# Kernel optimization log

Measured on AMD Instinct MI355X. Metric: run time of the kernel, lower is better.

Reference implementation:

```python
import jax, jax.numpy as jnp
import numpy as np

N_NODES = 50000

def _add_self_loops(edge_index, n):
    loop = jnp.arange(n, dtype=edge_index.dtype)
    src = jnp.concatenate([edge_index[0], loop])
    dst = jnp.concatenate([edge_index[1], loop])
    return src, dst

def _gcn_conv(x, src, dst, W, b, n):
    h = x @ W
    deg = jax.ops.segment_sum(jnp.ones_like(dst, dtype=h.dtype), dst, num_segments=n)
    inv_sqrt = jnp.where(deg > 0, jax.lax.rsqrt(deg), 0.0)
    coef = inv_sqrt[src] * inv_sqrt[dst]            # [E]
    msg = h[src] * coef[:, None]                     # [E, hidden]
    return jax.ops.segment_sum(msg, dst, num_segments=n) + b

def _gat_conv(x, src, dst, W, att_src, att_dst, b, n, heads, out_dim):
    # PyG GATConv, concat=False -> mean over heads; self-loops already added
    h = (x @ W).reshape(n, heads, out_dim)           # [N, H, F]
    a_src = jnp.sum(h * att_src, axis=-1)            # [N, H]
    a_dst = jnp.sum(h * att_dst, axis=-1)            # [N, H]
    e = a_src[src] + a_dst[dst]                      # [E, H]
    e = jax.nn.leaky_relu(e, negative_slope=0.2)
    # neighborhood softmax over edges grouped by destination
    m = jax.ops.segment_max(e, dst, num_segments=n)  # [N, H]
    ex = jnp.exp(e - m[dst])
    denom = jax.ops.segment_sum(ex, dst, num_segments=n)
    alpha = ex / denom[dst]                          # [E, H]
    out = jax.ops.segment_sum(h[src] * alpha[:, :, None], dst, num_segments=n)  # [N, H, F]
    return out.mean(axis=1) + b                      # concat=False -> head mean

def setup_inputs() -> dict:
    key = jax.random.key(0)
    ks = jax.random.split(key, 12)
    n, input_dim, hidden, output_dim, heads = N_NODES, 128, 128, 64, 2
    gat_out = hidden // 2
    x = jax.random.normal(ks[0], (n, input_dim), dtype=jnp.float32)
    edge_index = jax.random.randint(ks[1], (2, 800000), 0, n, dtype=jnp.int64)
    s = lambda fi, fo: float(np.sqrt(1.0 / fi))
    W1 = jax.random.normal(ks[2], (input_dim, hidden), dtype=jnp.float32) * s(input_dim, hidden)
    b1 = jnp.zeros((hidden,), dtype=jnp.float32)
    Wg = jax.random.normal(ks[3], (hidden, heads * gat_out), dtype=jnp.float32) * s(hidden, gat_out)
    att_src = jax.random.normal(ks[4], (heads, gat_out), dtype=jnp.float32) * s(gat_out, 1)
    att_dst = jax.random.normal(ks[5], (heads, gat_out), dtype=jnp.float32) * s(gat_out, 1)
    bg = jnp.zeros((gat_out,), dtype=jnp.float32)
    W3 = jax.random.normal(ks[6], (gat_out, output_dim), dtype=jnp.float32) * s(gat_out, output_dim)
    b3 = jnp.zeros((output_dim,), dtype=jnp.float32)
    return {"x": x, "edge_index": edge_index, "W1": W1, "b1": b1, "Wg": Wg,
            "att_src": att_src, "att_dst": att_dst, "bg": bg, "W3": W3, "b3": b3}

def reference(x, edge_index, W1, b1, Wg, att_src, att_dst, bg, W3, b3):
    n = x.shape[0]
    heads, gat_out = att_src.shape
    src, dst = _add_self_loops(edge_index, n)
    # dropout is identity in eval mode
    h = _gcn_conv(x, src, dst, W1, b1, n)
    h = jax.nn.relu(h)
    h = _gat_conv(h, src, dst, Wg, att_src, att_dst, bg, n, heads, gat_out)
    h = jax.nn.elu(h)
    return _gcn_conv(h, src, dst, W3, b3, n)
```

## Files before the change

kernel.cpp:

```cpp
#include <hip/hip_runtime.h>
#include <hip/hip_bf16.h>
#include <math.h>

#define N_NODES 50000
#define E0      800000
#define E_TOT   (E0 + N_NODES)
#define SCAP    512

using bf16 = __hip_bfloat16;
typedef __attribute__((ext_vector_type(8))) short bfrag;
typedef __attribute__((ext_vector_type(4))) float ffrag;

static __device__ __forceinline__ float bfu2f_lo(unsigned u){ return __uint_as_float(u << 16); }
static __device__ __forceinline__ float bfu2f_hi(unsigned u){ return __uint_as_float(u & 0xffff0000u); }

static __device__ __forceinline__ unsigned packbf(float a, float b){
    bf16 x = __float2bfloat16(a), y = __float2bfloat16(b);
    unsigned short ux = *reinterpret_cast<unsigned short*>(&x);
    unsigned short uy = *reinterpret_cast<unsigned short*>(&y);
    return ((unsigned)uy << 16) | ux;
}

static __device__ __forceinline__ int detect_f32(const unsigned* xu){
    int lane = threadIdx.x & 63;
    unsigned ex = (xu[lane] >> 7) & 0xFF;
    return (__ballot(ex < 100 || ex > 140) != 0ULL);
}
static __device__ __forceinline__ int detect_i32(const int* ei){
    int lane = threadIdx.x & 63;
    return (__ballot(ei[2 * lane + 1] != 0) != 0ULL);
}

static __device__ __forceinline__ float ldany(const void* p, int i, int isf32){
    return isf32 ? ((const float*)p)[i] : __bfloat162float(((const bf16*)p)[i]);
}

__global__ void k_convert(const void* __restrict__ xv,
                          const void* W1, const void* Wg, const void* W3,
                          const void* b1, const void* bg, const void* b3,
                          const void* as_, const void* ad_,
                          bf16* __restrict__ W1p, bf16* __restrict__ Wgp,
                          bf16* __restrict__ W3p, float* __restrict__ vecf,
                          bf16* __restrict__ xb, int* __restrict__ deg){
    const int NXB = (N_NODES * 32 + 255) / 256;
    int b = blockIdx.x, t = threadIdx.x;
    if (b >= 148 + NXB){
        int i = (b - 148 - NXB) * 256 + t;
        if (i < N_NODES) deg[i] = 0;
        return;
    }
    int isf = detect_f32((const unsigned*)xv);
    if (b >= 148){
        int i = (b - 148) * 256 + t;
        if (i < N_NODES * 32){
            if (isf){
                float4 v = ((const float4*)xv)[i];
                ((uint2*)xb)[i] = make_uint2(packbf(v.x, v.y), packbf(v.z, v.w));
            } else {
                ((uint2*)xb)[i] = ((const uint2*)xv)[i];
            }
        }
        return;
    }
    if (b < 16){
        int dd = b * 256 + t;
        int j  = dd & 7;
        int L  = (dd >> 3) & 63;
        int kc = (dd >> 9) & 1;
        int ct = dd >> 10;
        int k = kc * 32 + ((L >> 4) << 3) + j;
        int n = ct * 16 + (L & 15);
        W3p[dd] = __float2bfloat16(ldany(W3, k * 64 + n, isf));
    }
    else if (b < 18){
        int i = (b - 16) * 256 + t;
        float v;
        if      (i < 128) v = ldany(b1,  i,       isf);
        else if (i < 192) v = ldany(bg,  i - 128, isf);
        else if (i < 256) v = ldany(b3,  i - 192, isf);
        else if (i < 384) v = ldany(as_, i - 256, isf);
        else              v = ldany(ad_, i - 384, isf);
        vecf[i] = v;
    } else {
        int d = (b - 18) * 256 + t;
        const void* Wsrc = (d < 16384) ? W1 : Wg;
        bf16* Wdst = (d < 16384) ? W1p : Wgp;
        int dd = d & 16383;
        int j  = dd & 7;
        int L  = (dd >> 3) & 63;
        int kc = (dd >> 9) & 3;
        int ct = dd >> 11;
        int k = kc * 32 + ((L >> 4) << 3) + j;
        int n = ct * 16 + (L & 15);
        Wdst[dd] = __float2bfloat16(ldany(Wsrc, k * 128 + n, isf));
    }
}


static __device__ __forceinline__ int load_dst(const int* ei, int e, int is32){
    if (e >= E0) return e - E0;
    return is32 ? ei[E0 + e] : (int)((const long long*)ei)[E0 + e];
}
static __device__ __forceinline__ int load_src(const int* ei, int e, int is32){
    if (e >= E0) return e - E0;
    return is32 ? ei[e] : (int)((const long long*)ei)[e];
}

__global__ void k_count(const int* __restrict__ ei, int* __restrict__ deg,
                        int2* __restrict__ pkrk){
    int is32 = detect_i32(ei);
    int e = blockIdx.x * blockDim.x + threadIdx.x;
    if (e >= E_TOT) return;
    int dst = load_dst(ei, e, is32);
    int src = load_src(ei, e, is32);
    if ((unsigned)dst >= N_NODES || (unsigned)src >= N_NODES){
        pkrk[e] = make_int2(-1, 0);
        return;
    }
    int r = atomicAdd(&deg[dst], 1);
    pkrk[e] = make_int2((src << 16) | dst, r);
}

__global__ void k_scanA(const int* __restrict__ deg, int* __restrict__ tmp, int* __restrict__ blk){
    __shared__ int s[256];
    int t = threadIdx.x;
    int i = blockIdx.x * 256 + t;
    int v = (i < N_NODES) ? deg[i] : 0;
    s[t] = v; __syncthreads();
    for (int off = 1; off < 256; off <<= 1){
        int x = (t >= off) ? s[t - off] : 0;
        __syncthreads();
        s[t] += x;
        __syncthreads();
    }
    if (t == 255) blk[blockIdx.x] = s[255];
    if (i < N_NODES) tmp[i] = s[t] - v;
}

__global__ void k_scanC(int* __restrict__ row_ptr, const int* __restrict__ blk,
                        const int* __restrict__ deg, float* __restrict__ inv_sqrt,
                        int nb){
    __shared__ int s[256];
    int t = threadIdx.x;
    int B = blockIdx.x;
    s[t] = (t < nb && t < B) ? blk[t] : 0;
    __syncthreads();
    for (int off = 128; off; off >>= 1){
        if (t < off) s[t] += s[t + off];
        __syncthreads();
    }
    int base = s[0];
    int i = B * 256 + t;
    if (i < N_NODES){
        row_ptr[i] += base;
        int d = deg[i];
        inv_sqrt[i] = (d > 0) ? rsqrtf((float)d) : 0.0f;
    }
    if (i == 0) row_ptr[N_NODES] = E_TOT;
}

__global__ void k_fill(const int2* __restrict__ pkrk, const int* __restrict__ row_ptr,
                       const float* __restrict__ isq, int2* __restrict__ ecr){
    int e = blockIdx.x * blockDim.x + threadIdx.x;
    if (e >= E_TOT) return;
    int2 pr = pkrk[e];
    unsigned pk = (unsigned)pr.x;
    if (pk == 0xFFFFFFFFu) return;
    int dst = pk & 0xFFFF;
    int src = pk >> 16;
    int pos = row_ptr[dst] + pr.y;
    float c = isq[dst] * isq[src];
    ecr[pos] = make_int2(src, __float_as_int(c));
}

__global__ __launch_bounds__(256) void k_gather(
        const uint4* __restrict__ xb16, const int* __restrict__ rp,
        const int2* __restrict__ ecr, uint4* __restrict__ Xa16){
    __shared__ int   scsr[SCAP];
    __shared__ float scf[SCAP];
    int n0 = blockIdx.x * 4;
    int b0 = rp[n0];
    int stot = min(rp[n0 + 4] - b0, SCAP);
    for (int i = threadIdx.x; i < stot; i += 256){
        int2 ev = ecr[b0 + i];
        scsr[i] = ev.x;
        scf[i]  = __int_as_float(ev.y);
    }
    __syncthreads();

    int w = threadIdx.x >> 6, lane = threadIdx.x & 63;
    int q4 = lane >> 4, fz = lane & 15;
    int n = n0 + w;
    float a0=0,a1=0,a2=0,a3=0,a4=0,a5=0,a6=0,a7=0;
    int b = rp[n] - b0, e = rp[n + 1] - b0;
    int elim = min(e, stot);
    #pragma unroll 2
    for (int i = b + q4; i < elim; i += 4){
        int s = scsr[i];
        float c = scf[i];
        uint4 v = xb16[(size_t)s * 16 + fz];
        a0 += c * bfu2f_lo(v.x);  a1 += c * bfu2f_hi(v.x);
        a2 += c * bfu2f_lo(v.y);  a3 += c * bfu2f_hi(v.y);
        a4 += c * bfu2f_lo(v.z);  a5 += c * bfu2f_hi(v.z);
        a6 += c * bfu2f_lo(v.w);  a7 += c * bfu2f_hi(v.w);
    }
    int start = max(b, stot);
    int i0 = start + (((b + q4) - start) & 3);
    for (int i = i0; i < e; i += 4){
        int2 ev = ecr[b0 + i];
        float c = __int_as_float(ev.y);
        uint4 v = xb16[(size_t)ev.x * 16 + fz];
        a0 += c * bfu2f_lo(v.x);  a1 += c * bfu2f_hi(v.x);
        a2 += c * bfu2f_lo(v.y);  a3 += c * bfu2f_hi(v.y);
        a4 += c * bfu2f_lo(v.z);  a5 += c * bfu2f_hi(v.z);
        a6 += c * bfu2f_lo(v.w);  a7 += c * bfu2f_hi(v.w);
    }
    a0 += __shfl_xor(a0, 32, 64);  a0 += __shfl_xor(a0, 16, 64);
    a1 += __shfl_xor(a1, 32, 64);  a1 += __shfl_xor(a1, 16, 64);
    a2 += __shfl_xor(a2, 32, 64);  a2 += __shfl_xor(a2, 16, 64);
    a3 += __shfl_xor(a3, 32, 64);  a3 += __shfl_xor(a3, 16, 64);
    a4 += __shfl_xor(a4, 32, 64);  a4 += __shfl_xor(a4, 16, 64);
    a5 += __shfl_xor(a5, 32, 64);  a5 += __shfl_xor(a5, 16, 64);
    a6 += __shfl_xor(a6, 32, 64);  a6 += __shfl_xor(a6, 16, 64);
    a7 += __shfl_xor(a7, 32, 64);  a7 += __shfl_xor(a7, 16, 64);
    if (lane < 16){
        uint4 o;
        o.x = packbf(a0, a1);  o.y = packbf(a2, a3);
        o.z = packbf(a4, a5);  o.w = packbf(a6, a7);
        Xa16[(size_t)n * 16 + fz] = o;
    }
}

template<int EPI>
__global__ __launch_bounds__(512) void k_gemm_mfma(
        const bf16* __restrict__ A, const bf16* __restrict__ Wp,
        const float* __restrict__ vecf, bf16* __restrict__ O,
        float2* __restrict__ aS, float2* __restrict__ aD){
    int wid  = threadIdx.x >> 6;
    int lane = threadIdx.x & 63;
    int r0 = blockIdx.x * 128 + wid * 16;
    int m = lane & 15, q = lane >> 4;

    const bfrag* Ap = (const bfrag*)(A + (size_t)(r0 + m) * 128);
    bfrag af[4];
    #pragma unroll
    for (int kc = 0; kc < 4; ++kc) af[kc] = Ap[kc * 4 + q];

    ffrag c[8];
    #pragma unroll
    for (int ct = 0; ct < 8; ++ct){
        const bfrag* Bp = (const bfrag*)Wp + ct * 256 + lane;
        ffrag acc = {0.f, 0.f, 0.f, 0.f};
        #pragma unroll
        for (int kc = 0; kc < 4; ++kc)
            acc = __builtin_amdgcn_mfma_f32_16x16x32_bf16(af[kc], Bp[kc * 64], acc, 0, 0, 0);
        c[ct] = acc;
    }

    if (EPI == 0){
        #pragma unroll
        for (int ct = 0; ct < 8; ++ct){
            int col = ct * 16 + m;
            float bb = vecf[col];
            #pragma unroll
            for (int r = 0; r < 4; ++r){
                int row = r0 + q * 4 + r;
                if (row < N_NODES)
                    O[(size_t)row * 128 + col] = __float2bfloat16(fmaxf(c[ct][r] + bb, 0.f));
            }
        }
    } else {
        float ps0[4] = {0,0,0,0}, ps1[4] = {0,0,0,0};
        float pd0[4] = {0,0,0,0}, pd1[4] = {0,0,0,0};
        #pragma unroll
        for (int ct = 0; ct < 8; ++ct){
            const int h = ct >> 2;
            int f = (ct & 3) * 16 + m;
            float as_v = vecf[256 + h * 64 + f];
            float ad_v = vecf[384 + h * 64 + f];
            #pragma unroll
            for (int r = 0; r < 4; ++r){
                int row = r0 + q * 4 + r;
                if (row < N_NODES)
                    O[(size_t)row * 128 + f * 2 + h] = __float2bfloat16(c[ct][r]);
                if (h == 0){ ps0[r] += c[ct][r] * as_v;  pd0[r] += c[ct][r] * ad_v; }
                else       { ps1[r] += c[ct][r] * as_v;  pd1[r] += c[ct][r] * ad_v; }
            }
        }
        #pragma unroll
        for (int off = 1; off < 16; off <<= 1){
            #pragma unroll
            for (int r = 0; r < 4; ++r){
                ps0[r] += __shfl_xor(ps0[r], off, 64);
                ps1[r] += __shfl_xor(ps1[r], off, 64);
                pd0[r] += __shfl_xor(pd0[r], off, 64);
                pd1[r] += __shfl_xor(pd1[r], off, 64);
            }
        }
        if (m == 0){
            #pragma unroll
            for (int r = 0; r < 4; ++r){
                int row = r0 + q * 4 + r;
                if (row < N_NODES){
                    aS[row] = make_float2(ps0[r], ps1[r]);
                    aD[row] = make_float2(pd0[r], pd1[r]);
                }
            }
        }
    }
}

__global__ __launch_bounds__(256) void k_gemm_z(
        const bf16* __restrict__ Y, const bf16* __restrict__ W3p,
        bf16* __restrict__ Z){
    int wid  = threadIdx.x >> 6;
    int lane = threadIdx.x & 63;
    int r0 = blockIdx.x * 64 + wid * 16;
    int m = lane & 15, q = lane >> 4;

    const bfrag* Ap = (const bfrag*)(Y + (size_t)(r0 + m) * 64);
    bfrag af[2];
    #pragma unroll
    for (int kc = 0; kc < 2; ++kc) af[kc] = Ap[kc * 4 + q];

    #pragma unroll
    for (int ct = 0; ct < 4; ++ct){
        const bfrag* Bp = (const bfrag*)W3p + ct * 128 + lane;
        ffrag c = {0.f, 0.f, 0.f, 0.f};
        #pragma unroll
        for (int kc = 0; kc < 2; ++kc)
            c = __builtin_amdgcn_mfma_f32_16x16x32_bf16(af[kc], Bp[kc * 64], c, 0, 0, 0);
        int col = ct * 16 + m;
        #pragma unroll
        for (int r = 0; r < 4; ++r){
            int row = r0 + q * 4 + r;
            if (row < N_NODES)
                Z[(size_t)row * 64 + col] = __float2bfloat16(c[r]);
        }
    }
}

__global__ __launch_bounds__(256) void k_gat(
        const uint4* __restrict__ X2v, const int* __restrict__ rp,
        const int2* __restrict__ ecr, const float2* __restrict__ a_src,
        const float2* __restrict__ a_dst, const float* __restrict__ vecf,
        uint2* __restrict__ Yu2){
    __shared__ int    scsr[SCAP];
    __shared__ float2 pe[SCAP];
    int n0 = blockIdx.x * 4;
    int b0 = rp[n0];
    int stot = min(rp[n0 + 4] - b0, SCAP);
    for (int i = threadIdx.x; i < stot; i += 256) scsr[i] = ecr[b0 + i].x;
    __syncthreads();

    int w = threadIdx.x >> 6, lane = threadIdx.x & 63;
    int q4 = lane >> 4, fz = lane & 15;
    int n = n0 + w;
    float2 ad = a_dst[n];
    int b = rp[n] - b0, e = rp[n + 1] - b0;
    int elim = min(e, stot);

    for (int i = b + lane; i < elim; i += 64){
        float2 av = a_src[scsr[i]];
        float e0 = av.x + ad.x, e1 = av.y + ad.y;
        e0 = (e0 > 0.f) ? e0 : 0.2f * e0;
        e1 = (e1 > 0.f) ? e1 : 0.2f * e1;
        pe[i] = make_float2(__expf(e0), __expf(e1));
    }

    float l0 = 0.f, l1 = 0.f;
    float o00=0,o01=0, o10=0,o11=0, o20=0,o21=0, o30=0,o31=0;
    #pragma unroll 2
    for (int i = b + q4; i < elim; i += 4){
        float2 p = pe[i];
        uint4 v = X2v[(size_t)scsr[i] * 16 + fz];
        l0  += p.x;                  l1  += p.y;
        o00 += p.x * bfu2f_lo(v.x);  o01 += p.y * bfu2f_hi(v.x);
        o10 += p.x * bfu2f_lo(v.y);  o11 += p.y * bfu2f_hi(v.y);
        o20 += p.x * bfu2f_lo(v.z);  o21 += p.y * bfu2f_hi(v.z);
        o30 += p.x * bfu2f_lo(v.w);  o31 += p.y * bfu2f_hi(v.w);
    }
    int start = max(b, stot);
    int i0 = start + (((b + q4) - start) & 3);
    for (int i = i0; i < e; i += 4){
        int s = ecr[b0 + i].x;
        float2 av = a_src[s];
        uint4 v = X2v[(size_t)s * 16 + fz];
        float e0 = av.x + ad.x, e1 = av.y + ad.y;
        e0 = (e0 > 0.f) ? e0 : 0.2f * e0;
        e1 = (e1 > 0.f) ? e1 : 0.2f * e1;
        float p0 = __expf(e0), p1 = __expf(e1);
        l0  += p0;                 l1  += p1;
        o00 += p0 * bfu2f_lo(v.x); o01 += p1 * bfu2f_hi(v.x);
        o10 += p0 * bfu2f_lo(v.y); o11 += p1 * bfu2f_hi(v.y);
        o20 += p0 * bfu2f_lo(v.z); o21 += p1 * bfu2f_hi(v.z);
        o30 += p0 * bfu2f_lo(v.w); o31 += p1 * bfu2f_hi(v.w);
    }
    l0  += __shfl_xor(l0, 32, 64);   l0  += __shfl_xor(l0, 16, 64);
    l1  += __shfl_xor(l1, 32, 64);   l1  += __shfl_xor(l1, 16, 64);
    o00 += __shfl_xor(o00, 32, 64);  o00 += __shfl_xor(o00, 16, 64);
    o01 += __shfl_xor(o01, 32, 64);  o01 += __shfl_xor(o01, 16, 64);
    o10 += __shfl_xor(o10, 32, 64);  o10 += __shfl_xor(o10, 16, 64);
    o11 += __shfl_xor(o11, 32, 64);  o11 += __shfl_xor(o11, 16, 64);
    o20 += __shfl_xor(o20, 32, 64);  o20 += __shfl_xor(o20, 16, 64);
    o21 += __shfl_xor(o21, 32, 64);  o21 += __shfl_xor(o21, 16, 64);
    o30 += __shfl_xor(o30, 32, 64);  o30 += __shfl_xor(o30, 16, 64);
    o31 += __shfl_xor(o31, 32, 64);  o31 += __shfl_xor(o31, 16, 64);
    if (lane < 16){
        float v0 = 0.5f * (o00 / l0 + o01 / l1) + vecf[128 + 4 * fz + 0];
        float v1 = 0.5f * (o10 / l0 + o11 / l1) + vecf[128 + 4 * fz + 1];
        float v2 = 0.5f * (o20 / l0 + o21 / l1) + vecf[128 + 4 * fz + 2];
        float v3 = 0.5f * (o30 / l0 + o31 / l1) + vecf[128 + 4 * fz + 3];
        v0 = (v0 > 0.f) ? v0 : expm1f(v0);
        v1 = (v1 > 0.f) ? v1 : expm1f(v1);
        v2 = (v2 > 0.f) ? v2 : expm1f(v2);
        v3 = (v3 > 0.f) ? v3 : expm1f(v3);
        Yu2[(size_t)n * 16 + fz] = make_uint2(packbf(v0, v1), packbf(v2, v3));
    }
}

__global__ __launch_bounds__(256) void k_gather_out(
        const uint2* __restrict__ Zu2, const int* __restrict__ rp,
        const int2* __restrict__ ecr, const float* __restrict__ vecf,
        float4* __restrict__ out4){
    __shared__ int   scsr[SCAP];
    __shared__ float scf[SCAP];
    int n0 = blockIdx.x * 4;
    int b0 = rp[n0];
    int stot = min(rp[n0 + 4] - b0, SCAP);
    for (int i = threadIdx.x; i < stot; i += 256){
        int2 ev = ecr[b0 + i];
        scsr[i] = ev.x;
        scf[i]  = __int_as_float(ev.y);
    }
    __syncthreads();

    int w = threadIdx.x >> 6, lane = threadIdx.x & 63;
    int q4 = lane >> 4, fz = lane & 15;
    int n = n0 + w;
    float a0 = 0.f, a1 = 0.f, a2 = 0.f, a3 = 0.f;
    int b = rp[n] - b0, e = rp[n + 1] - b0;
    int elim = min(e, stot);
    #pragma unroll 2
    for (int i = b + q4; i < elim; i += 4){
        float c = scf[i];
        uint2 v = Zu2[(size_t)scsr[i] * 16 + fz];
        a0 += c * bfu2f_lo(v.x);  a1 += c * bfu2f_hi(v.x);
        a2 += c * bfu2f_lo(v.y);  a3 += c * bfu2f_hi(v.y);
    }
    int start = max(b, stot);
    int i0 = start + (((b + q4) - start) & 3);
    for (int i = i0; i < e; i += 4){
        int2 ev = ecr[b0 + i];
        float c = __int_as_float(ev.y);
        uint2 v = Zu2[(size_t)ev.x * 16 + fz];
        a0 += c * bfu2f_lo(v.x);  a1 += c * bfu2f_hi(v.x);
        a2 += c * bfu2f_lo(v.y);  a3 += c * bfu2f_hi(v.y);
    }
    a0 += __shfl_xor(a0, 32, 64);  a0 += __shfl_xor(a0, 16, 64);
    a1 += __shfl_xor(a1, 32, 64);  a1 += __shfl_xor(a1, 16, 64);
    a2 += __shfl_xor(a2, 32, 64);  a2 += __shfl_xor(a2, 16, 64);
    a3 += __shfl_xor(a3, 32, 64);  a3 += __shfl_xor(a3, 16, 64);
    if (lane < 16)
        out4[(size_t)n * 16 + fz] = make_float4(
            a0 + vecf[192 + 4 * fz + 0], a1 + vecf[192 + 4 * fz + 1],
            a2 + vecf[192 + 4 * fz + 2], a3 + vecf[192 + 4 * fz + 3]);
}


extern "C" void kernel_launch(void* const* d_in, const int* in_sizes, int n_in,
                              void* d_out, int out_size, void* d_ws, size_t ws_size,
                              hipStream_t stream) {
    const void* x  = d_in[0];
    const int*  ei = (const int*)d_in[1];
    float* out = (float*)d_out;

    char* p = (char*)d_ws;
    auto alloc = [&](size_t bytes) -> void* {
        void* r = (void*)p;
        p += (bytes + 255) & ~(size_t)255;
        return r;
    };
    int*   deg      = (int*)  alloc((size_t)N_NODES * 4);
    int*   row_ptr  = (int*)  alloc((size_t)(N_NODES + 1) * 4);
    int*   blk      = (int*)  alloc(256 * 4);
    int2*  pkrk     = (int2*) alloc((size_t)E_TOT * 8);
    int2*  ecr      = (int2*) alloc((size_t)E_TOT * 8);
    float* inv_sqrt = (float*)alloc((size_t)N_NODES * 4);
    float* a_src    = (float*)alloc((size_t)N_NODES * 2 * 4);
    float* a_dst    = (float*)alloc((size_t)N_NODES * 2 * 4);
    bf16*  W1p      = (bf16*) alloc(16384 * 2);
    bf16*  Wgp      = (bf16*) alloc(16384 * 2);
    bf16*  W3p      = (bf16*) alloc(4096 * 2);
    float* vecf     = (float*)alloc(512 * 4);
    bf16*  xb       = (bf16*) alloc((size_t)N_NODES * 128 * 2);
    bf16*  XA       = (bf16*) alloc((size_t)N_NODES * 128 * 2);
    bf16*  Y        = (bf16*) alloc((size_t)N_NODES * 64 * 2);
    bf16*  Z        = xb;

    const int NB_NODE = (N_NODES + 255) / 256;
    const int NB_EDGE = (E_TOT + 255) / 256;
    const int NXB     = (N_NODES * 32 + 255) / 256;
    const int NB_CONV = 148 + NXB + NB_NODE;
    const int NB_G128 = (N_NODES + 127) / 128;
    const int NB_G64  = (N_NODES + 63) / 64;

    k_convert<<<NB_CONV, 256, 0, stream>>>(x, d_in[2], d_in[4], d_in[8],
                                           d_in[3], d_in[7], d_in[9], d_in[5], d_in[6],
                                           W1p, Wgp, W3p, vecf, xb, deg);
    k_count<<<NB_EDGE, 256, 0, stream>>>(ei, deg, pkrk);
    k_scanA<<<NB_NODE, 256, 0, stream>>>(deg, row_ptr, blk);
    k_scanC<<<NB_NODE, 256, 0, stream>>>(row_ptr, blk, deg, inv_sqrt, NB_NODE);
    k_fill<<<NB_EDGE, 256, 0, stream>>>(pkrk, row_ptr, inv_sqrt, ecr);

    k_gather<<<N_NODES / 4, 256, 0, stream>>>((const uint4*)xb, row_ptr, ecr,
                                              (uint4*)XA);
    k_gemm_mfma<0><<<NB_G128, 512, 0, stream>>>(XA, W1p, vecf, XA,
                                                nullptr, nullptr);
    k_gemm_mfma<1><<<NB_G128, 512, 0, stream>>>(XA, Wgp, vecf, XA,
                                                (float2*)a_src, (float2*)a_dst);
    k_gat<<<N_NODES / 4, 256, 0, stream>>>((const uint4*)XA, row_ptr, ecr,
                                           (const float2*)a_src, (const float2*)a_dst,
                                           vecf, (uint2*)Y);
    k_gemm_z<<<NB_G64, 256, 0, stream>>>(Y, W3p, Z);
    k_gather_out<<<N_NODES / 4, 256, 0, stream>>>((const uint2*)Z, row_ptr, ecr,
                                                  vecf, (float4*)out);
}
```

Measured before the change: 271.5 us.

## Fuse the two dense GEMMs and fold the W3 projection into the final gather

```diff
diff --git a/kernel.cpp b/kernel.cpp
--- a/kernel.cpp
+++ b/kernel.cpp
@@ -40,7 +40,7 @@
                           const void* b1, const void* bg, const void* b3,
                           const void* as_, const void* ad_,
                           bf16* __restrict__ W1p, bf16* __restrict__ Wgp,
-                          bf16* __restrict__ W3p, float* __restrict__ vecf,
+                          bf16* __restrict__ W3r, float* __restrict__ vecf,
                           bf16* __restrict__ xb, int* __restrict__ deg){
     const int NXB = (N_NODES * 32 + 255) / 256;
     int b = blockIdx.x, t = threadIdx.x;
@@ -64,13 +64,7 @@
     }
     if (b < 16){
         int dd = b * 256 + t;
-        int j  = dd & 7;
-        int L  = (dd >> 3) & 63;
-        int kc = (dd >> 9) & 1;
-        int ct = dd >> 10;
-        int k = kc * 32 + ((L >> 4) << 3) + j;
-        int n = ct * 16 + (L & 15);
-        W3p[dd] = __float2bfloat16(ldany(W3, k * 64 + n, isf));
+        W3r[dd] = __float2bfloat16(ldany(W3, dd, isf));
     }
     else if (b < 18){
         int i = (b - 16) * 256 + t;
@@ -231,111 +225,85 @@
     }
 }
 
-template<int EPI>
-__global__ __launch_bounds__(512) void k_gemm_mfma(
-        const bf16* __restrict__ A, const bf16* __restrict__ Wp,
-        const float* __restrict__ vecf, bf16* __restrict__ O,
-        float2* __restrict__ aS, float2* __restrict__ aD){
+__global__ __launch_bounds__(512) void k_gemm2(
+        const bf16* __restrict__ A, const bf16* __restrict__ W1p,
+        const bf16* __restrict__ Wgp, const float* __restrict__ vecf,
+        bf16* __restrict__ O, float2* __restrict__ aS, float2* __restrict__ aD){
+    __shared__ __align__(16) unsigned char lds[8][4096];
     int wid  = threadIdx.x >> 6;
     int lane = threadIdx.x & 63;
     int r0 = blockIdx.x * 128 + wid * 16;
     int m = lane & 15, q = lane >> 4;
+    unsigned char* myl = lds[wid];
 
     const bfrag* Ap = (const bfrag*)(A + (size_t)(r0 + m) * 128);
     bfrag af[4];
     #pragma unroll
     for (int kc = 0; kc < 4; ++kc) af[kc] = Ap[kc * 4 + q];
 
-    ffrag c[8];
     #pragma unroll
     for (int ct = 0; ct < 8; ++ct){
-        const bfrag* Bp = (const bfrag*)Wp + ct * 256 + lane;
+        const bfrag* Bp = (const bfrag*)W1p + ct * 256 + lane;
         ffrag acc = {0.f, 0.f, 0.f, 0.f};
         #pragma unroll
         for (int kc = 0; kc < 4; ++kc)
             acc = __builtin_amdgcn_mfma_f32_16x16x32_bf16(af[kc], Bp[kc * 64], acc, 0, 0, 0);
-        c[ct] = acc;
-    }
-
-    if (EPI == 0){
+        int col = ct * 16 + m;
+        float bb = vecf[col];
         #pragma unroll
-        for (int ct = 0; ct < 8; ++ct){
-            int col = ct * 16 + m;
-            float bb = vecf[col];
-            #pragma unroll
-            for (int r = 0; r < 4; ++r){
-                int row = r0 + q * 4 + r;
-                if (row < N_NODES)
-                    O[(size_t)row * 128 + col] = __float2bfloat16(fmaxf(c[ct][r] + bb, 0.f));
-            }
+        for (int r = 0; r < 4; ++r){
+            int row = q * 4 + r;
+            unsigned byte = (unsigned)(row * 256 + col * 2) ^ ((row & 7) << 4);
+            *(bf16*)(myl + byte) = __float2bfloat16(fmaxf(acc[r] + bb, 0.f));
         }
-    } else {
-        float ps0[4] = {0,0,0,0}, ps1[4] = {0,0,0,0};
-        float pd0[4] = {0,0,0,0}, pd1[4] = {0,0,0,0};
+    }
+    bfrag af2[4];
+    #pragma unroll
+    for (int kc = 0; kc < 4; ++kc){
+        unsigned byte = (unsigned)(m * 256 + (kc * 32 + q * 8) * 2) ^ ((m & 7) << 4);
+        af2[kc] = *(const bfrag*)(myl + byte);
+    }
+
+    float ps0[4] = {0,0,0,0}, ps1[4] = {0,0,0,0};
+    float pd0[4] = {0,0,0,0}, pd1[4] = {0,0,0,0};
+    #pragma unroll
+    for (int ct = 0; ct < 8; ++ct){
+        const bfrag* Bp = (const bfrag*)Wgp + ct * 256 + lane;
+        ffrag acc = {0.f, 0.f, 0.f, 0.f};
         #pragma unroll
-        for (int ct = 0; ct < 8; ++ct){
-            const int h = ct >> 2;
-            int f = (ct & 3) * 16 + m;
-            float as_v = vecf[256 + h * 64 + f];
-            float ad_v = vecf[384 + h * 64 + f];
-            #pragma unroll
-            for (int r = 0; r < 4; ++r){
-                int row = r0 + q * 4 + r;
-                if (row < N_NODES)
-                    O[(size_t)row * 128 + f * 2 + h] = __float2bfloat16(c[ct][r]);
-                if (h == 0){ ps0[r] += c[ct][r] * as_v;  pd0[r] += c[ct][r] * ad_v; }
-                else       { ps1[r] += c[ct][r] * as_v;  pd1[r] += c[ct][r] * ad_v; }
-            }
-        }
-        #pragma unroll
-        for (int off = 1; off < 16; off <<= 1){
-            #pragma unroll
-            for (int r = 0; r < 4; ++r){
-                ps0[r] += __shfl_xor(ps0[r], off, 64);
-                ps1[r] += __shfl_xor(ps1[r], off, 64);
-                pd0[r] += __shfl_xor(pd0[r], off, 64);
-                pd1[r] += __shfl_xor(pd1[r], off, 64);
-            }
-        }
-        if (m == 0){
-            #pragma unroll
-            for (int r = 0; r < 4; ++r){
-                int row = r0 + q * 4 + r;
-                if (row < N_NODES){
-                    aS[row] = make_float2(ps0[r], ps1[r]);
-                    aD[row] = make_float2(pd0[r], pd1[r]);
-                }
-            }
-        }
-    }
-}
-
-__global__ __launch_bounds__(256) void k_gemm_z(
-        const bf16* __restrict__ Y, const bf16* __restrict__ W3p,
-        bf16* __restrict__ Z){
-    int wid  = threadIdx.x >> 6;
-    int lane = threadIdx.x & 63;
-    int r0 = blockIdx.x * 64 + wid * 16;
-    int m = lane & 15, q = lane >> 4;
-
-    const bfrag* Ap = (const bfrag*)(Y + (size_t)(r0 + m) * 64);
-    bfrag af[2];
-    #pragma unroll
-    for (int kc = 0; kc < 2; ++kc) af[kc] = Ap[kc * 4 + q];
-
-    #pragma unroll
-    for (int ct = 0; ct < 4; ++ct){
-        const bfrag* Bp = (const bfrag*)W3p + ct * 128 + lane;
-        ffrag c = {0.f, 0.f, 0.f, 0.f};
-        #pragma unroll
-        for (int kc = 0; kc < 2; ++kc)
-            c = __builtin_amdgcn_mfma_f32_16x16x32_bf16(af[kc], Bp[kc * 64], c, 0, 0, 0);
-        int col = ct * 16 + m;
+        for (int kc = 0; kc < 4; ++kc)
+            acc = __builtin_amdgcn_mfma_f32_16x16x32_bf16(af2[kc], Bp[kc * 64], acc, 0, 0, 0);
+        const int h = ct >> 2;
+        int f = (ct & 3) * 16 + m;
+        float as_v = vecf[256 + h * 64 + f];
+        float ad_v = vecf[384 + h * 64 + f];
         #pragma unroll
         for (int r = 0; r < 4; ++r){
             int row = r0 + q * 4 + r;
             if (row < N_NODES)
-                Z[(size_t)row * 64 + col] = __float2bfloat16(c[r]);
+                O[(size_t)row * 128 + f * 2 + h] = __float2bfloat16(acc[r]);
+            if (h == 0){ ps0[r] += acc[r] * as_v;  pd0[r] += acc[r] * ad_v; }
+            else       { ps1[r] += acc[r] * as_v;  pd1[r] += acc[r] * ad_v; }
+        }
+    }
+    #pragma unroll
+    for (int off = 1; off < 16; off <<= 1){
+        #pragma unroll
+        for (int r = 0; r < 4; ++r){
+            ps0[r] += __shfl_xor(ps0[r], off, 64);
+            ps1[r] += __shfl_xor(ps1[r], off, 64);
+            pd0[r] += __shfl_xor(pd0[r], off, 64);
+            pd1[r] += __shfl_xor(pd1[r], off, 64);
+        }
+    }
+    if (m == 0){
+        #pragma unroll
+        for (int r = 0; r < 4; ++r){
+            int row = r0 + q * 4 + r;
+            if (row < N_NODES){
+                aS[row] = make_float2(ps0[r], ps1[r]);
+                aD[row] = make_float2(pd0[r], pd1[r]);
+            }
         }
     }
 }
@@ -420,11 +388,13 @@
 }
 
 __global__ __launch_bounds__(256) void k_gather_out(
-        const uint2* __restrict__ Zu2, const int* __restrict__ rp,
-        const int2* __restrict__ ecr, const float* __restrict__ vecf,
-        float4* __restrict__ out4){
+        const uint2* __restrict__ Yu2, const int* __restrict__ rp,
+        const int2* __restrict__ ecr, const bf16* __restrict__ W3r,
+        const float* __restrict__ vecf, float* __restrict__ out){
     __shared__ int   scsr[SCAP];
     __shared__ float scf[SCAP];
+    __shared__ bf16  sW3[4096];
+    __shared__ float sagg[4][64];
     int n0 = blockIdx.x * 4;
     int b0 = rp[n0];
     int stot = min(rp[n0 + 4] - b0, SCAP);
@@ -432,6 +402,12 @@
         int2 ev = ecr[b0 + i];
         scsr[i] = ev.x;
         scf[i]  = __int_as_float(ev.y);
+    }
+    {
+        uint4* d = (uint4*)sW3;
+        const uint4* s = (const uint4*)W3r;
+        d[threadIdx.x]       = s[threadIdx.x];
+        d[threadIdx.x + 256] = s[threadIdx.x + 256];
     }
     __syncthreads();
 
@@ -444,7 +420,7 @@
     #pragma unroll 2
     for (int i = b + q4; i < elim; i += 4){
         float c = scf[i];
-        uint2 v = Zu2[(size_t)scsr[i] * 16 + fz];
+        uint2 v = Yu2[(size_t)scsr[i] * 16 + fz];
         a0 += c * bfu2f_lo(v.x);  a1 += c * bfu2f_hi(v.x);
         a2 += c * bfu2f_lo(v.y);  a3 += c * bfu2f_hi(v.y);
     }
@@ -453,7 +429,7 @@
     for (int i = i0; i < e; i += 4){
         int2 ev = ecr[b0 + i];
         float c = __int_as_float(ev.y);
-        uint2 v = Zu2[(size_t)ev.x * 16 + fz];
+        uint2 v = Yu2[(size_t)ev.x * 16 + fz];
         a0 += c * bfu2f_lo(v.x);  a1 += c * bfu2f_hi(v.x);
         a2 += c * bfu2f_lo(v.y);  a3 += c * bfu2f_hi(v.y);
     }
@@ -462,9 +438,15 @@
     a2 += __shfl_xor(a2, 32, 64);  a2 += __shfl_xor(a2, 16, 64);
     a3 += __shfl_xor(a3, 32, 64);  a3 += __shfl_xor(a3, 16, 64);
     if (lane < 16)
-        out4[(size_t)n * 16 + fz] = make_float4(
-            a0 + vecf[192 + 4 * fz + 0], a1 + vecf[192 + 4 * fz + 1],
-            a2 + vecf[192 + 4 * fz + 2], a3 + vecf[192 + 4 * fz + 3]);
+        ((float4*)sagg[w])[fz] = make_float4(a0, a1, a2, a3);
+
+    int f = lane;
+    float acc = vecf[192 + f];
+    const float* ag = sagg[w];
+    #pragma unroll 8
+    for (int k = 0; k < 64; ++k)
+        acc += ag[k] * __bfloat162float(sW3[k * 64 + f]);
+    out[(size_t)n * 64 + f] = acc;
 }
 
 
@@ -491,23 +473,21 @@
     float* a_dst    = (float*)alloc((size_t)N_NODES * 2 * 4);
     bf16*  W1p      = (bf16*) alloc(16384 * 2);
     bf16*  Wgp      = (bf16*) alloc(16384 * 2);
-    bf16*  W3p      = (bf16*) alloc(4096 * 2);
+    bf16*  W3r      = (bf16*) alloc(4096 * 2);
     float* vecf     = (float*)alloc(512 * 4);
     bf16*  xb       = (bf16*) alloc((size_t)N_NODES * 128 * 2);
     bf16*  XA       = (bf16*) alloc((size_t)N_NODES * 128 * 2);
     bf16*  Y        = (bf16*) alloc((size_t)N_NODES * 64 * 2);
-    bf16*  Z        = xb;
 
     const int NB_NODE = (N_NODES + 255) / 256;
     const int NB_EDGE = (E_TOT + 255) / 256;
     const int NXB     = (N_NODES * 32 + 255) / 256;
     const int NB_CONV = 148 + NXB + NB_NODE;
     const int NB_G128 = (N_NODES + 127) / 128;
-    const int NB_G64  = (N_NODES + 63) / 64;
 
     k_convert<<<NB_CONV, 256, 0, stream>>>(x, d_in[2], d_in[4], d_in[8],
                                            d_in[3], d_in[7], d_in[9], d_in[5], d_in[6],
-                                           W1p, Wgp, W3p, vecf, xb, deg);
+                                           W1p, Wgp, W3r, vecf, xb, deg);
     k_count<<<NB_EDGE, 256, 0, stream>>>(ei, deg, pkrk);
     k_scanA<<<NB_NODE, 256, 0, stream>>>(deg, row_ptr, blk);
     k_scanC<<<NB_NODE, 256, 0, stream>>>(row_ptr, blk, deg, inv_sqrt, NB_NODE);
@@ -515,14 +495,11 @@
 
     k_gather<<<N_NODES / 4, 256, 0, stream>>>((const uint4*)xb, row_ptr, ecr,
                                               (uint4*)XA);
-    k_gemm_mfma<0><<<NB_G128, 512, 0, stream>>>(XA, W1p, vecf, XA,
-                                                nullptr, nullptr);
-    k_gemm_mfma<1><<<NB_G128, 512, 0, stream>>>(XA, Wgp, vecf, XA,
-                                                (float2*)a_src, (float2*)a_dst);
+    k_gemm2<<<NB_G128, 512, 0, stream>>>(XA, W1p, Wgp, vecf, XA,
+                                         (float2*)a_src, (float2*)a_dst);
     k_gat<<<N_NODES / 4, 256, 0, stream>>>((const uint4*)XA, row_ptr, ecr,
                                            (const float2*)a_src, (const float2*)a_dst,
                                            vecf, (uint2*)Y);
-    k_gemm_z<<<NB_G64, 256, 0, stream>>>(Y, W3p, Z);
-    k_gather_out<<<N_NODES / 4, 256, 0, stream>>>((const uint2*)Z, row_ptr, ecr,
-                                                  vecf, (float4*)out);
-}
+    k_gather_out<<<N_NODES / 4, 256, 0, stream>>>((const uint2*)Y, row_ptr, ecr,
+                                                  W3r, vecf, out);
+}
```

New measurement: 267.7 us. Within noise of the previous version (-1.4%).
